# Performance work log

Hardware: AMD Instinct MI355X
Metric: run time of the kernel (lower is better)

Reference implementation:

```python
import jax, jax.numpy as jnp
import numpy as np

EPS = 1e-8


def setup_inputs() -> dict:
    key = jax.random.key(0)
    ks = jax.random.split(key, 8)
    B, N, D = 8, 2048, 768
    H, R = 768, 4
    return {
        "x": jax.random.normal(ks[0], (B, N, D), dtype=jnp.float32),
        "scale": jnp.ones((D,), dtype=jnp.float32),
        "U": jax.random.normal(ks[1], (H, R), dtype=jnp.float32) * 0.02,
        "V": jax.random.normal(ks[2], (H, R), dtype=jnp.float32) * 0.02,
        "S_param": jax.random.normal(ks[3], (H, H), dtype=jnp.float32) * 0.01,
        "Bm": jax.random.normal(ks[4], (H, D), dtype=jnp.float32) * (1.0 / np.sqrt(D)),
        "Cm": jax.random.normal(ks[5], (D, H), dtype=jnp.float32) * (1.0 / np.sqrt(H)),
        "gate_w": jax.random.normal(ks[6], (D, D), dtype=jnp.float32) * (1.0 / np.sqrt(D)),
        "gate_b": jnp.zeros((D,), dtype=jnp.float32),
        "alpha": jnp.full((1,), 0.1, dtype=jnp.float32),
    }


def reference(x, scale, U, V, S_param, Bm, Cm, gate_w, gate_b, alpha):
    B, N, D = x.shape
    H = Bm.shape[0]
    # A = diag(A_diag) + U V^T + (S - S^T); A_diag is a fixed buffer.
    A_diag = -jnp.linspace(1.0, float(H), H, dtype=x.dtype) / H
    A = jnp.diag(A_diag) + U @ V.T + (S_param - S_param.T)
    At = A.T  # apply as h @ A.T
    # RMSNorm
    rms = jnp.sqrt(jnp.mean(x * x, axis=-1, keepdims=True) + EPS)
    xn = x / rms * scale
    # Precompute input injections u_t = x_t @ B.T for all t: (N, B, H)
    u = jnp.einsum('bnd,hd->nbh', xn, Bm)

    def step(h, ut):
        h = h @ At + ut
        return h, h @ Cm.T  # (B, D)

    h0 = jnp.zeros((B, H), dtype=x.dtype)
    _, y_fwd = jax.lax.scan(step, h0, u)                 # (N, B, D)
    _, y_bwd = jax.lax.scan(step, h0, u, reverse=True)   # (N, B, D), indexed in time order
    y = 0.5 * (y_fwd + y_bwd)
    y = jnp.swapaxes(y, 0, 1)  # (B, N, D)
    # Gate
    g = jax.nn.sigmoid(jnp.einsum('bnd,ed->bne', xn, gate_w) + gate_b)
    y = y * g
    # Skip (dropout is identity in eval)
    return x + alpha * y
```

## Files before the change

### kernel.cpp

```cpp
#include <hip/hip_runtime.h>


typedef short  bfrag __attribute__((ext_vector_type(8)));
typedef float  ffrag __attribute__((ext_vector_type(4)));
typedef float  f4    __attribute__((ext_vector_type(4)));
typedef short  s4v   __attribute__((ext_vector_type(4)));

#define DEV static __device__ __forceinline__
#define Hn 768
#define FLS 132
#define BLS 260

DEV unsigned short f2bf(float f) {
  unsigned u = __float_as_uint(f);
  u += 0x7fffu + ((u >> 16) & 1u);
  return (unsigned short)(u >> 16);
}
DEV float bf2f(unsigned short s) { return __uint_as_float(((unsigned)s) << 16); }

DEV ffrag mfma16(bfrag a, bfrag b, ffrag c) {
  return __builtin_amdgcn_mfma_f32_16x16x32_bf16(a, b, c, 0, 0, 0);
}

DEV void glds16(const unsigned short* g, unsigned short* l) {
  __builtin_amdgcn_global_load_lds(
      (const __attribute__((address_space(1))) unsigned int*)g,
      (__attribute__((address_space(3))) unsigned int*)l, 16, 0, 0);
}

union BF8 { bfrag v; unsigned short u[8]; };

__global__ __launch_bounds__(256) void k_abuild(
    const float* __restrict__ U, const float* __restrict__ V,
    const float* __restrict__ S, const float* __restrict__ Bm,
    const float* __restrict__ Cm, const float* __restrict__ gw,
    float* __restrict__ Af, float* __restrict__ AfT,
    unsigned short* __restrict__ Abf,
    unsigned short* __restrict__ Bmb, unsigned short* __restrict__ Cmb,
    unsigned short* __restrict__ gwb, unsigned short* __restrict__ zp) {
  int i = blockIdx.x;
  int task = blockIdx.y;
  if (task == 0) {
    float u0 = U[i*4+0], u1 = U[i*4+1], u2 = U[i*4+2], u3 = U[i*4+3];
    for (int j = threadIdx.x; j < Hn; j += 256) {
      float a = u0*V[j*4+0] + u1*V[j*4+1] + u2*V[j*4+2] + u3*V[j*4+3]
              + S[i*Hn+j] - S[j*Hn+i];
      if (i == j) a += -(float)(i+1) / 768.0f;
      Af[i*Hn+j]  = a;
      AfT[j*Hn+i] = a;
      Abf[i*Hn+j] = f2bf(a);
    }
    if (i == 0) for (int j = threadIdx.x; j < 1024; j += 256) zp[j] = 0;
  } else {
    const float* src = (task==1) ? Bm : (task==2) ? Cm : gw;
    unsigned short* dst = (task==1) ? Bmb : (task==2) ? Cmb : gwb;
    for (int j = threadIdx.x; j < Hn; j += 256) dst[i*Hn+j] = f2bf(src[i*Hn+j]);
  }
}

__global__ __launch_bounds__(256) void k_rms(
    const float* __restrict__ x, const float* __restrict__ scale,
    unsigned short* __restrict__ xn) {
  int row  = blockIdx.x * 4 + (threadIdx.x >> 6);
  int lane = threadIdx.x & 63;
  int b = row >> 11, t = row & 2047;
  const float* xr = x + (long)row * Hn;
  float v[12];
  float ss = 0.f;
#pragma unroll
  for (int j = 0; j < 12; ++j) { v[j] = xr[lane + j*64]; ss += v[j]*v[j]; }
#pragma unroll
  for (int off = 1; off < 64; off <<= 1) ss += __shfl_xor(ss, off);
  float inv = 1.0f / sqrtf(ss / 768.0f + 1e-8f);
  unsigned short* dst = xn + ((long)t * 8 + b) * Hn;
#pragma unroll
  for (int j = 0; j < 12; ++j) dst[lane + j*64] = f2bf(v[j] * inv * scale[lane + j*64]);
}

__global__ __launch_bounds__(256) void k_sq(
    const float* __restrict__ X, const float* __restrict__ XT,
    float* __restrict__ Z, float* __restrict__ ZT,
    unsigned short* __restrict__ Zbf) {
  int tid = threadIdx.x, lane = tid & 63, w = tid >> 6;
  int mw = w >> 1, nw = w & 1, l15 = lane & 15, lhi = lane >> 4;
  int rb = blockIdx.x * 64, cb = blockIdx.y * 64;
  ffrag acc[2][2] = {};
  for (int kt = 0; kt < 24; ++kt) {
    int k0 = kt*32 + lhi*8;
    BF8 ah[2], al[2], bh[2], bl[2];
#pragma unroll
    for (int mt = 0; mt < 2; ++mt) {
      const f4* p = (const f4*)(X + (long)(rb + mw*32 + mt*16 + l15) * Hn + k0);
      f4 x0 = p[0], x1 = p[1];
#pragma unroll
      for (int j = 0; j < 8; ++j) {
        float f = (j < 4) ? x0[j] : x1[j-4];
        unsigned short h = f2bf(f);
        ah[mt].u[j] = h; al[mt].u[j] = f2bf(f - bf2f(h));
      }
    }
#pragma unroll
    for (int nt = 0; nt < 2; ++nt) {
      const f4* p = (const f4*)(XT + (long)(cb + nw*32 + nt*16 + l15) * Hn + k0);
      f4 x0 = p[0], x1 = p[1];
#pragma unroll
      for (int j = 0; j < 8; ++j) {
        float f = (j < 4) ? x0[j] : x1[j-4];
        unsigned short h = f2bf(f);
        bh[nt].u[j] = h; bl[nt].u[j] = f2bf(f - bf2f(h));
      }
    }
#pragma unroll
    for (int mt = 0; mt < 2; ++mt)
#pragma unroll
      for (int nt = 0; nt < 2; ++nt) {
        acc[mt][nt] = mfma16(ah[mt].v, bh[nt].v, acc[mt][nt]);
        acc[mt][nt] = mfma16(ah[mt].v, bl[nt].v, acc[mt][nt]);
        acc[mt][nt] = mfma16(al[mt].v, bh[nt].v, acc[mt][nt]);
      }
  }
#pragma unroll
  for (int mt = 0; mt < 2; ++mt)
#pragma unroll
    for (int nt = 0; nt < 2; ++nt)
#pragma unroll
      for (int q = 0; q < 4; ++q) {
        int grow = rb + mw*32 + mt*16 + lhi*4 + q;
        int gcol = cb + nw*32 + nt*16 + l15;
        float vv = acc[mt][nt][q];
        Z[(long)grow*Hn + gcol] = vv;
        ZT[(long)gcol*Hn + grow] = vv;
        Zbf[(long)grow*Hn + gcol] = f2bf(vv);
      }
}

template<int MODE>
__global__ __launch_bounds__(512) void k_lvl(
    const unsigned short* __restrict__ A0s, const unsigned short* __restrict__ B0s,
    const unsigned short* __restrict__ res, unsigned short* __restrict__ outb,
    const unsigned short* __restrict__ zp, int sh) {
  constexpr int NS   = (MODE == 2) ? 2 : 1;
  constexpr int BUFS = NS * 4096 + 8192;
  __shared__ __align__(16) unsigned short ldsb[2 * BUFS];

  const int tid = threadIdx.x, lane = tid & 63, w = tid >> 6;
  const int l15 = lane & 15, lhi = lane >> 4;
  const int wr = w >> 2, wc = w & 3;

  const int nwg = gridDim.x;
  const int q8 = nwg >> 3, r8 = nwg & 7, xcd = blockIdx.x & 7, fo = blockIdx.x >> 3;
  const int wg = (xcd < r8 ? xcd*(q8+1) : r8*(q8+1) + (xcd - r8)*q8) + fo;
  const int cb = wg % 3, rbk = wg / 3;
  const long r0  = (long)rbk * 128;
  const long bc0 = (long)cb * 256;
  const int dir = (MODE == 1 && r0 >= 16384) ? 1 : 0;

  bool skip = false;
  if (MODE == 1)
    skip = dir ? (r0 >= 32768 - sh) : (r0 + 128 <= sh);

  const int rowin = lane >> 2, ch = lane & 3;
  const int rA = w*16 + rowin;
  const int cswz = ch ^ ((rowin ^ (rowin >> 2)) & 3);
  long gA[NS]; bool vA[NS];
#pragma unroll
  for (int s = 0; s < NS; ++s) {
    long gr; bool ok = true;
    if (MODE == 0) {
      gr = r0 + rA;
    } else if (MODE == 1) {
      gr = r0 + rA + (dir ? sh : -sh);
      ok = dir ? (gr < 32768) : (gr >= 0);
    } else {
      if (s == 0) { gr = r0 + rA - sh;         ok = (gr >= 0);    }
      else        { gr = r0 + rA + 16384 + sh; ok = (gr < 32768); }
    }
    vA[s] = ok; gA[s] = gr * Hn + cswz*8;
  }
  long gB[2];
#pragma unroll
  for (int j = 0; j < 2; ++j)
    gB[j] = (bc0 + j*128 + rA) * Hn + cswz*8;

  auto stage = [&](int buf, int kt) {
    const int ko = kt * 32;
    unsigned short* dst = ldsb + buf * BUFS;
#pragma unroll
    for (int s = 0; s < NS; ++s) {
      const unsigned short* g = vA[s] ? (A0s + gA[s] + ko) : zp;
      glds16(g, dst + s*4096 + w*512);
    }
#pragma unroll
    for (int j = 0; j < 2; ++j)
      glds16(B0s + gB[j] + ko, dst + NS*4096 + j*4096 + w*512);
  };

  ffrag acc[4][4] = {};
  const int cx = (lhi ^ ((l15 ^ (l15 >> 2)) & 3)) * 8;

  if (!skip) {
    stage(0, 0);
    __syncthreads();
    int cur = 0;
    for (int kt = 0; kt < 24; ++kt) {
      if (kt < 23) stage(cur ^ 1, kt + 1);
      const unsigned short* L = ldsb + cur * BUFS;
      bfrag a[NS][4], b[4];
#pragma unroll
      for (int mt = 0; mt < 4; ++mt) {
        const int row = wr*64 + mt*16 + l15;
#pragma unroll
        for (int s = 0; s < NS; ++s)
          a[s][mt] = *(const bfrag*)&L[s*4096 + row*32 + cx];
      }
#pragma unroll
      for (int nt = 0; nt < 4; ++nt) {
        const int row = wc*64 + nt*16 + l15;
        b[nt] = *(const bfrag*)&L[NS*4096 + row*32 + cx];
      }
#pragma unroll
      for (int mt = 0; mt < 4; ++mt)
#pragma unroll
        for (int nt = 0; nt < 4; ++nt) {
          acc[mt][nt] = mfma16(a[0][mt], b[nt], acc[mt][nt]);
          if (NS == 2) acc[mt][nt] = mfma16(a[1][mt], b[nt], acc[mt][nt]);
        }
      __syncthreads();
      cur ^= 1;
    }
  }

  float* fl = (float*)ldsb;
#pragma unroll
  for (int p = 0; p < 4; ++p) {
    __syncthreads();
#pragma unroll
    for (int nt = 0; nt < 4; ++nt)
#pragma unroll
      for (int q = 0; q < 4; ++q)
        fl[(wr*16 + lhi*4 + q)*BLS + wc*64 + nt*16 + l15] = acc[p][nt][q];
    __syncthreads();
    for (int i = tid; i < 2048; i += 512) {
      const int srow = i >> 6;
      const int cc   = (i & 63) << 2;
      f4 v = *(const f4*)&fl[srow*BLS + cc];
      const long grow = r0 + (srow >> 4)*64 + p*16 + (srow & 15);
      const long gcol = bc0 + cc;
      const long go = grow * Hn + gcol;
      if (MODE == 0) {
        s4v ov;
#pragma unroll
        for (int j = 0; j < 4; ++j) ((unsigned short*)&ov)[j] = f2bf(v[j]);
        *(s4v*)&outb[go] = ov;
        *(s4v*)&outb[go + (long)16384*Hn] = ov;
      } else if (MODE == 1) {
        s4v rv = *(const s4v*)&res[go];
#pragma unroll
        for (int j = 0; j < 4; ++j) v[j] += bf2f(((unsigned short*)&rv)[j]);
        s4v ov;
#pragma unroll
        for (int j = 0; j < 4; ++j) ((unsigned short*)&ov)[j] = f2bf(v[j]);
        *(s4v*)&outb[go] = ov;
      } else {
        s4v ra = *(const s4v*)&res[go];
        s4v rb2 = *(const s4v*)&res[go + (long)16384*Hn];
#pragma unroll
        for (int j = 0; j < 4; ++j)
          v[j] += bf2f(((unsigned short*)&ra)[j]) + bf2f(((unsigned short*)&rb2)[j]);
        s4v ov;
#pragma unroll
        for (int j = 0; j < 4; ++j) ((unsigned short*)&ov)[j] = f2bf(v[j]);
        *(s4v*)&outb[go] = ov;
      }
    }
  }
}

__global__ __launch_bounds__(256) void k_fin(
    const unsigned short* __restrict__ A0s, const unsigned short* __restrict__ A1s,
    const unsigned short* __restrict__ B0s, const unsigned short* __restrict__ B1s,
    const unsigned short* __restrict__ zp,
    const float* __restrict__ gb, const float* __restrict__ alpha,
    const float* __restrict__ x, float* __restrict__ outf) {
  __shared__ __align__(16) char smem[2 * 4 * 8192];
  unsigned short* ldsb = (unsigned short*)smem;

  const int tid = threadIdx.x, lane = tid & 63, w = tid >> 6;
  const int l15 = lane & 15, lhi = lane >> 4;
  const int wr = w >> 1, wc = w & 1;

  const int nwg = gridDim.x;
  const int q8 = nwg >> 3, r8 = nwg & 7, xcd = blockIdx.x & 7, fo = blockIdx.x >> 3;
  const int wg = (xcd < r8 ? xcd*(q8+1) : r8*(q8+1) + (xcd - r8)*q8) + fo;
  const int cb = wg % 6, rbk = wg / 6;
  const long r0 = (long)rbk * 128;
  const long bc0 = (long)cb * 128;

  const int rowin = lane >> 2, ch = lane & 3;
  long gA[2][2]; long gB[2][2]; int lbase[2];
#pragma unroll
  for (int jj = 0; jj < 2; ++jj) {
    const int inst = w*2 + jj;
    const int r = inst*16 + rowin;
    const int c = ch ^ ((r ^ (r >> 2)) & 3);
    lbase[jj] = inst * 512;
    gA[0][jj] = (r0 + r) * Hn + c*8;
    gA[1][jj] = gA[0][jj];
    gB[0][jj] = (bc0 + r) * Hn + c*8;
    gB[1][jj] = gB[0][jj];
  }

  auto stage = [&](int buf, int kt) {
    const int ko = kt * 32;
    unsigned short* dst = ldsb + buf * 16384;
#pragma unroll
    for (int jj = 0; jj < 2; ++jj) {
      glds16(A0s + gA[0][jj] + ko, dst + 0*4096 + lbase[jj]);
      glds16(A1s + gA[1][jj] + ko, dst + 1*4096 + lbase[jj]);
      glds16(B0s + gB[0][jj] + ko, dst + 2*4096 + lbase[jj]);
      glds16(B1s + gB[1][jj] + ko, dst + 3*4096 + lbase[jj]);
    }
  };

  ffrag acc[4][4] = {};
  ffrag accZ[4][4] = {};
  const int cx = (lhi ^ ((l15 ^ (l15 >> 2)) & 3)) * 8;

  stage(0, 0);
  int cur = 0;
  for (int kt = 0; kt < 24; ++kt) {
    asm volatile("s_waitcnt vmcnt(0)" ::: "memory");
    __builtin_amdgcn_s_barrier();
    if (kt < 23) stage(cur ^ 1, kt + 1);
    const unsigned short* L = ldsb + cur * 16384;
    bfrag a[2][4], b0[4], b1[4];
#pragma unroll
    for (int mt = 0; mt < 4; ++mt) {
      const int row = wr*64 + mt*16 + l15;
      a[0][mt] = *(const bfrag*)&L[row*32 + cx];
      a[1][mt] = *(const bfrag*)&L[4096 + row*32 + cx];
    }
#pragma unroll
    for (int nt = 0; nt < 4; ++nt) {
      const int row = wc*64 + nt*16 + l15;
      b0[nt] = *(const bfrag*)&L[2*4096 + row*32 + cx];
      b1[nt] = *(const bfrag*)&L[3*4096 + row*32 + cx];
    }
#pragma unroll
    for (int mt = 0; mt < 4; ++mt)
#pragma unroll
      for (int nt = 0; nt < 4; ++nt) {
        acc[mt][nt]  = mfma16(a[0][mt], b0[nt], acc[mt][nt]);
        accZ[mt][nt] = mfma16(a[1][mt], b1[nt], accZ[mt][nt]);
      }
    cur ^= 1;
  }

  const float al = alpha[0];
  float gvals[4];
#pragma unroll
  for (int nt = 0; nt < 4; ++nt) gvals[nt] = gb[bc0 + wc*64 + nt*16 + l15];
#pragma unroll
  for (int mt = 0; mt < 4; ++mt)
#pragma unroll
    for (int nt = 0; nt < 4; ++nt)
#pragma unroll
      for (int q = 0; q < 4; ++q) {
        float z = accZ[mt][nt][q] + gvals[nt];
        float g = 1.0f / (1.0f + __expf(-z));
        acc[mt][nt][q] *= al * 0.5f * g;
      }

  float* fl = (float*)smem;
#pragma unroll
  for (int hh = 0; hh < 2; ++hh) {
    __syncthreads();
    if (wr == hh) {
#pragma unroll
      for (int mt = 0; mt < 4; ++mt)
#pragma unroll
        for (int nt = 0; nt < 4; ++nt)
#pragma unroll
          for (int q = 0; q < 4; ++q)
            fl[(mt*16 + lhi*4 + q)*FLS + wc*64 + nt*16 + l15] = acc[mt][nt][q];
    }
    __syncthreads();
    for (int i = tid; i < 2048; i += 256) {
      const int row = i >> 5;
      const int cc  = (i & 31) << 2;
      f4 v = *(const f4*)&fl[row*FLS + cc];
      const long grow = r0 + hh*64 + row;
      const long gcol = bc0 + cc;
      const long t = grow >> 3, b = grow & 7;
      const long o = (b*2048 + t)*Hn + gcol;
      f4 xv = *(const f4*)&x[o];
      f4 ov;
#pragma unroll
      for (int j = 0; j < 4; ++j) ov[j] = xv[j] + v[j];
      *(f4*)&outf[o] = ov;
    }
  }
}

extern "C" void kernel_launch(void* const* d_in, const int* in_sizes, int n_in,
                              void* d_out, int out_size, void* d_ws, size_t ws_size,
                              hipStream_t stream) {
  const float* x     = (const float*)d_in[0];
  const float* scale = (const float*)d_in[1];
  const float* U     = (const float*)d_in[2];
  const float* V     = (const float*)d_in[3];
  const float* S     = (const float*)d_in[4];
  const float* Bm    = (const float*)d_in[5];
  const float* Cm    = (const float*)d_in[6];
  const float* gw    = (const float*)d_in[7];
  const float* gb    = (const float*)d_in[8];
  const float* alpha = (const float*)d_in[9];
  float* out = (float*)d_out;

  char* p = (char*)d_ws;
  auto alloc = [&](size_t sz) { char* r = p; p += (sz + 255) & ~(size_t)255; return r; };

  const size_t SZ_X  = (size_t)32768 * Hn * sizeof(unsigned short);
  const size_t SZ_BF = (size_t)16384 * Hn * sizeof(unsigned short);
  const size_t SZ_M  = (size_t)Hn * Hn * sizeof(float);
  const size_t SZ_MB = (size_t)Hn * Hn * sizeof(unsigned short);

  unsigned short* xn = (unsigned short*)alloc(SZ_BF);
  unsigned short* XA = (unsigned short*)alloc(SZ_X);
  unsigned short* XB = (unsigned short*)alloc(SZ_X);
  float* Af  = (float*)alloc(SZ_M);
  float* AfT = (float*)alloc(SZ_M);
  float* P1  = (float*)alloc(SZ_M);
  float* P1T = (float*)alloc(SZ_M);
  float* P2  = (float*)alloc(SZ_M);
  float* P2T = (float*)alloc(SZ_M);
  unsigned short* Abf = (unsigned short*)alloc(SZ_MB);
  unsigned short* Ab[10];
  for (int i = 0; i < 10; ++i) Ab[i] = (unsigned short*)alloc(SZ_MB);
  unsigned short* Bmb = (unsigned short*)alloc(SZ_MB);
  unsigned short* Cmb = (unsigned short*)alloc(SZ_MB);
  unsigned short* gwb = (unsigned short*)alloc(SZ_MB);
  unsigned short* zp  = (unsigned short*)alloc(1024 * sizeof(unsigned short));

  if ((size_t)(p - (char*)d_ws) > ws_size) return;

  k_abuild<<<dim3(768, 4), 256, 0, stream>>>(U, V, S, Bm, Cm, gw,
      Af, AfT, Abf, Bmb, Cmb, gwb, zp);
  k_rms<<<4096, 256, 0, stream>>>(x, scale, xn);

  const float* sx = Af; const float* sxt = AfT;
  float* za = P1; float* zat = P1T; float* zb = P2; float* zbt = P2T;
  for (int i = 0; i < 10; ++i) {
    k_sq<<<dim3(12, 12), 256, 0, stream>>>(sx, sxt, za, zat, Ab[i]);
    sx = za; sxt = zat;
    float* t1 = za; float* t2 = zat; za = zb; zat = zbt; zb = t1; zbt = t2;
  }

  k_lvl<0><<<384, 512, 0, stream>>>(xn, Bmb, nullptr, XA, zp, 0);

  unsigned short* src = XA; unsigned short* dst = XB;
  for (int i = 0; i < 10; ++i) {
    const unsigned short* W = (i == 0) ? Abf : Ab[i-1];
    k_lvl<1><<<768, 512, 0, stream>>>(src, W, src, dst, zp, 8 << i);
    unsigned short* t = src; src = dst; dst = t;
  }
  k_lvl<2><<<384, 512, 0, stream>>>(src, Ab[9], src, XB, zp, 8192);

  k_fin<<<768, 256, 0, stream>>>(XB, xn, Cmb, gwb, zp, gb, alpha, x, out);
}
```

Before: 1.227 ms.

## Switch prefix-scan from radix-2 doubling to radix-4 levels with fused powers

Replaces the ten radix-2 scan levels, each a separate k_lvl launch adding one shifted term times a matrix power, with five radix-4 levels. Each new level accumulates three shifted terms against A^s, A^2s and A^3s inside one kernel. The extra powers (A^3, A^12, A^48, and so on) come from batched two-matrix k_mul launches. This halves the number of level passes over the 32768x768 activation buffer and the launches, at the cost of three GEMM chains per level and more power-matrix products. Since the k-loop per level triples, total MFMA work is similar or higher, and the saving comes mostly from fewer full read/write sweeps.

```diff
diff --git a/kernel.cpp b/kernel.cpp
--- a/kernel.cpp
+++ b/kernel.cpp
@@ -77,10 +77,17 @@
   for (int j = 0; j < 12; ++j) dst[lane + j*64] = f2bf(v[j] * inv * scale[lane + j*64]);
 }
 
-__global__ __launch_bounds__(256) void k_sq(
-    const float* __restrict__ X, const float* __restrict__ XT,
-    float* __restrict__ Z, float* __restrict__ ZT,
-    unsigned short* __restrict__ Zbf) {
+__global__ __launch_bounds__(256) void k_mul(
+    const float* __restrict__ X0, const float* __restrict__ Y0T,
+    float* __restrict__ Z0, float* __restrict__ Z0T, unsigned short* __restrict__ Zb0,
+    const float* __restrict__ X1, const float* __restrict__ Y1T,
+    float* __restrict__ Z1, float* __restrict__ Z1T, unsigned short* __restrict__ Zb1) {
+  const float* X  = blockIdx.z ? X1 : X0;
+  const float* YT = blockIdx.z ? Y1T : Y0T;
+  float* Z  = blockIdx.z ? Z1 : Z0;
+  float* ZT = blockIdx.z ? Z1T : Z0T;
+  unsigned short* Zb = blockIdx.z ? Zb1 : Zb0;
+
   int tid = threadIdx.x, lane = tid & 63, w = tid >> 6;
   int mw = w >> 1, nw = w & 1, l15 = lane & 15, lhi = lane >> 4;
   int rb = blockIdx.x * 64, cb = blockIdx.y * 64;
@@ -101,7 +108,7 @@
     }
 #pragma unroll
     for (int nt = 0; nt < 2; ++nt) {
-      const f4* p = (const f4*)(XT + (long)(cb + nw*32 + nt*16 + l15) * Hn + k0);
+      const f4* p = (const f4*)(YT + (long)(cb + nw*32 + nt*16 + l15) * Hn + k0);
       f4 x0 = p[0], x1 = p[1];
 #pragma unroll
       for (int j = 0; j < 8; ++j) {
@@ -128,15 +135,16 @@
         int grow = rb + mw*32 + mt*16 + lhi*4 + q;
         int gcol = cb + nw*32 + nt*16 + l15;
         float vv = acc[mt][nt][q];
-        Z[(long)grow*Hn + gcol] = vv;
-        ZT[(long)gcol*Hn + grow] = vv;
-        Zbf[(long)grow*Hn + gcol] = f2bf(vv);
+        if (Z)  Z[(long)grow*Hn + gcol] = vv;
+        if (ZT) ZT[(long)gcol*Hn + grow] = vv;
+        Zb[(long)grow*Hn + gcol] = f2bf(vv);
       }
 }
 
 template<int MODE>
 __global__ __launch_bounds__(512) void k_lvl(
     const unsigned short* __restrict__ A0s, const unsigned short* __restrict__ B0s,
+    const unsigned short* __restrict__ B1s, const unsigned short* __restrict__ B2s,
     const unsigned short* __restrict__ res, unsigned short* __restrict__ outb,
     const unsigned short* __restrict__ zp, int sh) {
   constexpr int NS   = (MODE == 2) ? 2 : 1;
@@ -153,10 +161,10 @@
   const int cb = wg % 3, rbk = wg / 3;
   const long r0  = (long)rbk * 128;
   const long bc0 = (long)cb * 256;
-  const int dir = (MODE == 1 && r0 >= 16384) ? 1 : 0;
+  const int dir = (MODE == 3 && r0 >= 16384) ? 1 : 0;
 
   bool skip = false;
-  if (MODE == 1)
+  if (MODE == 3)
     skip = dir ? (r0 >= 32768 - sh) : (r0 + 128 <= sh);
 
   const int rowin = lane >> 2, ch = lane & 3;
@@ -166,17 +174,23 @@
 #pragma unroll
   for (int s = 0; s < NS; ++s) {
     long gr; bool ok = true;
-    if (MODE == 0) {
+    if (MODE == 0 || MODE == 3) {
       gr = r0 + rA;
-    } else if (MODE == 1) {
-      gr = r0 + rA + (dir ? sh : -sh);
-      ok = dir ? (gr < 32768) : (gr >= 0);
     } else {
       if (s == 0) { gr = r0 + rA - sh;         ok = (gr >= 0);    }
       else        { gr = r0 + rA + 16384 + sh; ok = (gr < 32768); }
     }
     vA[s] = ok; gA[s] = gr * Hn + cswz*8;
   }
+  long gA3[3]; bool vA3[3];
+  if (MODE == 3) {
+#pragma unroll
+    for (int s = 0; s < 3; ++s) {
+      long gr = r0 + rA + (dir ? (long)(s+1)*sh : -(long)(s+1)*sh);
+      vA3[s] = dir ? (gr < 32768) : (gr >= 0);
+      gA3[s] = gr * Hn + cswz*8;
+    }
+  }
   long gB[2];
 #pragma unroll
   for (int j = 0; j < 2; ++j)
@@ -195,10 +209,49 @@
       glds16(B0s + gB[j] + ko, dst + NS*4096 + j*4096 + w*512);
   };
 
+  auto stage3 = [&](int buf, int s, int kt) {
+    const int ko = kt * 32;
+    unsigned short* dst = ldsb + buf * BUFS;
+    const unsigned short* g = vA3[s] ? (A0s + gA3[s] + ko) : zp;
+    glds16(g, dst + w*512);
+    const unsigned short* Bs = (s == 0) ? B0s : (s == 1) ? B1s : B2s;
+#pragma unroll
+    for (int j = 0; j < 2; ++j)
+      glds16(Bs + gB[j] + ko, dst + 4096 + j*4096 + w*512);
+  };
+
   ffrag acc[4][4] = {};
   const int cx = (lhi ^ ((l15 ^ (l15 >> 2)) & 3)) * 8;
 
-  if (!skip) {
+  if (MODE == 3) {
+    if (!skip) {
+      stage3(0, 0, 0);
+      __syncthreads();
+      int cur = 0;
+#pragma unroll
+      for (int s = 0; s < 3; ++s) {
+        for (int kt = 0; kt < 24; ++kt) {
+          if (kt < 23)      stage3(cur ^ 1, s, kt + 1);
+          else if (s < 2)   stage3(cur ^ 1, s + 1, 0);
+          const unsigned short* L = ldsb + cur * BUFS;
+          bfrag a[4], b[4];
+#pragma unroll
+          for (int mt = 0; mt < 4; ++mt)
+            a[mt] = *(const bfrag*)&L[(wr*64 + mt*16 + l15)*32 + cx];
+#pragma unroll
+          for (int nt = 0; nt < 4; ++nt)
+            b[nt] = *(const bfrag*)&L[4096 + (wc*64 + nt*16 + l15)*32 + cx];
+#pragma unroll
+          for (int mt = 0; mt < 4; ++mt)
+#pragma unroll
+            for (int nt = 0; nt < 4; ++nt)
+              acc[mt][nt] = mfma16(a[mt], b[nt], acc[mt][nt]);
+          __syncthreads();
+          cur ^= 1;
+        }
+      }
+    }
+  } else {
     stage(0, 0);
     __syncthreads();
     int cur = 0;
@@ -253,7 +306,7 @@
         for (int j = 0; j < 4; ++j) ((unsigned short*)&ov)[j] = f2bf(v[j]);
         *(s4v*)&outb[go] = ov;
         *(s4v*)&outb[go + (long)16384*Hn] = ov;
-      } else if (MODE == 1) {
+      } else if (MODE == 3) {
         s4v rv = *(const s4v*)&res[go];
 #pragma unroll
         for (int j = 0; j < 4; ++j) v[j] += bf2f(((unsigned short*)&rv)[j]);
@@ -430,13 +483,15 @@
   unsigned short* XB = (unsigned short*)alloc(SZ_X);
   float* Af  = (float*)alloc(SZ_M);
   float* AfT = (float*)alloc(SZ_M);
-  float* P1  = (float*)alloc(SZ_M);
-  float* P1T = (float*)alloc(SZ_M);
-  float* P2  = (float*)alloc(SZ_M);
-  float* P2T = (float*)alloc(SZ_M);
+  float* K0  = (float*)alloc(SZ_M);  float* K0T = (float*)alloc(SZ_M);
+  float* K1  = (float*)alloc(SZ_M);  float* K1T = (float*)alloc(SZ_M);
+  float* K2  = (float*)alloc(SZ_M);  float* K2T = (float*)alloc(SZ_M);
   unsigned short* Abf = (unsigned short*)alloc(SZ_MB);
-  unsigned short* Ab[10];
-  for (int i = 0; i < 10; ++i) Ab[i] = (unsigned short*)alloc(SZ_MB);
+  unsigned short* Pb[15];
+  for (int i = 0; i < 15; ++i) Pb[i] = (unsigned short*)alloc(SZ_MB);
+  unsigned short* A2b=Pb[0],*A3b=Pb[1],*A4b=Pb[2],*A8b=Pb[3],*A12b=Pb[4],
+      *A16b=Pb[5],*A32b=Pb[6],*A48b=Pb[7],*A64b=Pb[8],*A128b=Pb[9],
+      *A192b=Pb[10],*A256b=Pb[11],*A512b=Pb[12],*A768b=Pb[13],*A1024b=Pb[14];
   unsigned short* Bmb = (unsigned short*)alloc(SZ_MB);
   unsigned short* Cmb = (unsigned short*)alloc(SZ_MB);
   unsigned short* gwb = (unsigned short*)alloc(SZ_MB);
@@ -448,23 +503,39 @@
       Af, AfT, Abf, Bmb, Cmb, gwb, zp);
   k_rms<<<4096, 256, 0, stream>>>(x, scale, xn);
 
-  const float* sx = Af; const float* sxt = AfT;
-  float* za = P1; float* zat = P1T; float* zb = P2; float* zbt = P2T;
-  for (int i = 0; i < 10; ++i) {
-    k_sq<<<dim3(12, 12), 256, 0, stream>>>(sx, sxt, za, zat, Ab[i]);
-    sx = za; sxt = zat;
-    float* t1 = za; float* t2 = zat; za = zb; zat = zbt; zb = t1; zbt = t2;
-  }
-
-  k_lvl<0><<<384, 512, 0, stream>>>(xn, Bmb, nullptr, XA, zp, 0);
-
-  unsigned short* src = XA; unsigned short* dst = XB;
-  for (int i = 0; i < 10; ++i) {
-    const unsigned short* W = (i == 0) ? Abf : Ab[i-1];
-    k_lvl<1><<<768, 512, 0, stream>>>(src, W, src, dst, zp, 8 << i);
-    unsigned short* t = src; src = dst; dst = t;
-  }
-  k_lvl<2><<<384, 512, 0, stream>>>(src, Ab[9], src, XB, zp, 8192);
-
-  k_fin<<<768, 256, 0, stream>>>(XB, xn, Cmb, gwb, zp, gb, alpha, x, out);
-}
+  dim3 g1(12, 12, 1), g2(12, 12, 2);
+  k_mul<<<g1, 256, 0, stream>>>(Af, AfT, K0, K0T, A2b,
+                                nullptr, nullptr, nullptr, nullptr, nullptr);
+  k_mul<<<g2, 256, 0, stream>>>(Af, K0T, nullptr, nullptr, A3b,
+                                K0, K0T, K1, K1T, A4b);
+  k_mul<<<g1, 256, 0, stream>>>(K1, K1T, K2, K2T, A8b,
+                                nullptr, nullptr, nullptr, nullptr, nullptr);
+  k_mul<<<g2, 256, 0, stream>>>(K1, K2T, nullptr, nullptr, A12b,
+                                K2, K2T, K0, K0T, A16b);
+  k_mul<<<g1, 256, 0, stream>>>(K0, K0T, K1, K1T, A32b,
+                                nullptr, nullptr, nullptr, nullptr, nullptr);
+  k_mul<<<g2, 256, 0, stream>>>(K0, K1T, nullptr, nullptr, A48b,
+                                K1, K1T, K2, K2T, A64b);
+  k_mul<<<g1, 256, 0, stream>>>(K2, K2T, K0, K0T, A128b,
+                                nullptr, nullptr, nullptr, nullptr, nullptr);
+  k_mul<<<g2, 256, 0, stream>>>(K2, K0T, nullptr, nullptr, A192b,
+                                K0, K0T, K1, K1T, A256b);
+  k_mul<<<g1, 256, 0, stream>>>(K1, K1T, K2, K2T, A512b,
+                                nullptr, nullptr, nullptr, nullptr, nullptr);
+  k_mul<<<g2, 256, 0, stream>>>(K1, K2T, nullptr, nullptr, A768b,
+                                K2, K2T, nullptr, nullptr, A1024b);
+
+  k_lvl<0><<<384, 512, 0, stream>>>(xn, Bmb, nullptr, nullptr,
+      nullptr, XA, zp, 0);
+
+  k_lvl<3><<<768, 512, 0, stream>>>(XA, Abf,   A2b,   A3b,   XA, XB, zp, 8);
+  k_lvl<3><<<768, 512, 0, stream>>>(XB, A4b,   A8b,   A12b,  XB, XA, zp, 32);
+  k_lvl<3><<<768, 512, 0, stream>>>(XA, A16b,  A32b,  A48b,  XA, XB, zp, 128);
+  k_lvl<3><<<768, 512, 0, stream>>>(XB, A64b,  A128b, A192b, XB, XA, zp, 512);
+  k_lvl<3><<<768, 512, 0, stream>>>(XA, A256b, A512b, A768b, XA, XB, zp, 2048);
+
+  k_lvl<2><<<384, 512, 0, stream>>>(XB, A1024b, nullptr, nullptr,
+      XB, XA, zp, 8192);
+
+  k_fin<<<768, 256, 0, stream>>>(XA, xn, Cmb, gwb, zp, gb, alpha, x, out);
+}
```

Measured after the change: 1.340 ms. +9.2%, slower.
